# Optimization experiments

Measured on AMD Instinct MI355X. Metric: run time of the kernel, lower is better.

## Reference

```python
import jax, jax.numpy as jnp
import numpy as np

T, N, D, H = 512, 64, 1024, 1024  # time, batch(envs), input dim, hidden dim


def setup_inputs() -> dict:
    key = jax.random.key(0)
    ks = jax.random.split(key, 7)
    x = jax.random.normal(ks[0], (T, N, D), jnp.float32)
    hx = jax.random.normal(ks[1], (N, H), jnp.float32)
    mask = (jax.random.uniform(ks[2], (T, N)) > 0.05).astype(jnp.float32)
    s = float(1.0 / np.sqrt(H))
    w_ih = jax.random.uniform(ks[3], (3 * H, D), jnp.float32, -s, s)
    w_hh = jax.random.uniform(ks[4], (3 * H, H), jnp.float32, -s, s)
    b_ih = jax.random.uniform(ks[5], (3 * H,), jnp.float32, -s, s)
    b_hh = jax.random.uniform(ks[6], (3 * H,), jnp.float32, -s, s)
    return {"x": x, "hx": hx, "mask": mask, "w_ih": w_ih, "w_hh": w_hh,
            "b_ih": b_ih, "b_hh": b_hh}


def reference(x, hx, mask, w_ih, w_hh, b_ih, b_hh):
    """Masked GRU scan, equivalent to the segment-splitting torch loop:
    h is multiplied by mask[t] before every step (mask==1 inside episodes,
    0 at episode boundaries, so this matches masking only at segment starts).
    """
    # Precompute input projections for all timesteps in one big GEMM: [T,N,3H]
    gi = jnp.einsum('tnd,gd->tng', x, w_ih) + b_ih

    def step(h, inp):
        gi_t, m_t = inp                       # [N,3H], [N]
        h = h * m_t[:, None]                  # reset hidden at episode starts
        gh = h @ w_hh.T + b_hh                # [N,3H]
        i_r, i_z, i_n = jnp.split(gi_t, 3, axis=-1)
        h_r, h_z, h_n = jnp.split(gh, 3, axis=-1)
        r = jax.nn.sigmoid(i_r + h_r)
        z = jax.nn.sigmoid(i_z + h_z)
        n = jnp.tanh(i_n + r * h_n)
        h_new = (1.0 - z) * n + z * h
        return h_new, h_new

    h_final, out = jax.lax.scan(step, hx, (gi, mask))
    return out, h_final
```

## Files before the change

kernel.cpp:

```cpp
#include <hip/hip_runtime.h>

#define TT 512
#define NN 64
#define DD 1024
#define HH 1024
#define NSLOT 32

typedef __attribute__((ext_vector_type(8))) short bf16x8;
typedef __attribute__((ext_vector_type(4))) float f32x4;
typedef __attribute__((ext_vector_type(8))) unsigned short u16x8;
typedef __attribute__((ext_vector_type(4))) int i32x4;
typedef __attribute__((ext_vector_type(2))) int i32x2;

__device__ unsigned short g_wih[192u * 2048 * 8];
__device__ unsigned short g_whh[192u * 2048 * 8];
__device__ unsigned short g_x[2048u * 2048 * 8];
__device__ unsigned short g_gi[(size_t)2048 * 64 * 768];
__device__ unsigned g_hbuf32[(size_t)NSLOT * 4 * 16384];

__device__ __forceinline__ unsigned short f2bf(float f) {
  unsigned u = __float_as_uint(f);
  u += 0x7fffu + ((u >> 16) & 1u);
  return (unsigned short)(u >> 16);
}

__global__ void prep_kernel(const float* __restrict__ x,
                            const float* __restrict__ wih,
                            const float* __restrict__ whh) {
  const int gsz = gridDim.x * blockDim.x;
  const int gid = blockIdx.x * blockDim.x + threadIdx.x;
  for (int z = gid; z < NSLOT * 4 * 16384; z += gsz) g_hbuf32[z] = 0u;

  const int W8 = 192 * 2048;
  const int X8 = 2048 * 2048;
  for (int idx = gid; idx < 2 * W8 + X8; idx += gsz) {
    if (idx < 2 * W8) {
      const float* src = (idx < W8) ? wih : whh;
      unsigned short* dst = (idx < W8) ? g_wih : g_whh;
      int i8 = (idx < W8) ? idx : idx - W8;
      size_t g = (size_t)i8 * 8;
      int col = (int)(g >> 10);
      int k = (int)(g & 1023);
      int kk = k >> 5, lg = (k >> 3) & 3;
      int cg = col >> 4;
      int l = (col & 15) | (lg << 4);
      size_t o8 = ((size_t)cg * 32 + kk) * 64 + l;
      const float* p = src + g;
      float4 v0 = *(const float4*)(p);
      float4 v1 = *(const float4*)(p + 4);
      u16x8 u;
      u[0] = f2bf(v0.x); u[1] = f2bf(v0.y); u[2] = f2bf(v0.z); u[3] = f2bf(v0.w);
      u[4] = f2bf(v1.x); u[5] = f2bf(v1.y); u[6] = f2bf(v1.z); u[7] = f2bf(v1.w);
      *(u16x8*)(dst + o8 * 8) = u;
    } else {
      int i8 = idx - 2 * W8;
      size_t g = (size_t)i8 * 8;
      int row = (int)(g >> 10);
      int k = (int)(g & 1023);
      int t = row >> 6, env = row & 63;
      int eg = env >> 4;
      int kk = k >> 5, lg = (k >> 3) & 3;
      int l = (env & 15) | (lg << 4);
      size_t o8 = (((size_t)t * 4 + eg) * 32 + kk) * 64 + l;
      const float* p = x + g;
      float4 v0 = *(const float4*)(p);
      float4 v1 = *(const float4*)(p + 4);
      u16x8 u;
      u[0] = f2bf(v0.x); u[1] = f2bf(v0.y); u[2] = f2bf(v0.z); u[3] = f2bf(v0.w);
      u[4] = f2bf(v1.x); u[5] = f2bf(v1.y); u[6] = f2bf(v1.z); u[7] = f2bf(v1.w);
      *(u16x8*)(g_x + o8 * 8) = u;
    }
  }
}

__global__ __launch_bounds__(256) void gemm_gi() {
  extern __shared__ char smem[];
  unsigned short* As = (unsigned short*)smem;
  unsigned short* Bs = As + 2048 * 8;
  const int tid = threadIdx.x;
  const int bid = blockIdx.x;
  const int mblk = bid & 255, nblk = bid >> 8;
  const int w = tid >> 6, l = tid & 63;
  const int wm = w >> 1, wn = w & 1;

  u16x8 pa[8], pb[8];
  #pragma unroll
  for (int i = 0; i < 8; ++i) {
    int e = tid + i * 256;
    int mt = e >> 8, kkl = (e >> 6) & 3, lane = e & 63;
    pa[i] = *((const u16x8*)g_x  + ((size_t)(mblk * 8 + mt) * 32 + kkl) * 64 + lane);
    pb[i] = *((const u16x8*)g_wih + ((size_t)(nblk * 8 + mt) * 32 + kkl) * 64 + lane);
  }
  f32x4 acc[4][4] = {};
  for (int c = 0; c < 8; ++c) {
    __syncthreads();
    #pragma unroll
    for (int i = 0; i < 8; ++i) {
      int e = tid + i * 256;
      ((u16x8*)As)[e] = pa[i];
      ((u16x8*)Bs)[e] = pb[i];
    }
    __syncthreads();
    if (c < 7) {
      #pragma unroll
      for (int i = 0; i < 8; ++i) {
        int e = tid + i * 256;
        int mt = e >> 8, kkl = (e >> 6) & 3, lane = e & 63;
        pa[i] = *((const u16x8*)g_x  + ((size_t)(mblk * 8 + mt) * 32 + (c + 1) * 4 + kkl) * 64 + lane);
        pb[i] = *((const u16x8*)g_wih + ((size_t)(nblk * 8 + mt) * 32 + (c + 1) * 4 + kkl) * 64 + lane);
      }
    }
    #pragma unroll
    for (int kkl = 0; kkl < 4; ++kkl) {
      bf16x8 af[4], bfr[4];
      #pragma unroll
      for (int ai = 0; ai < 4; ++ai) af[ai]  = ((const bf16x8*)As)[((wm * 4 + ai) * 4 + kkl) * 64 + l];
      #pragma unroll
      for (int bi = 0; bi < 4; ++bi) bfr[bi] = ((const bf16x8*)Bs)[((wn * 4 + bi) * 4 + kkl) * 64 + l];
      #pragma unroll
      for (int ai = 0; ai < 4; ++ai)
        #pragma unroll
        for (int bi = 0; bi < 4; ++bi)
          acc[ai][bi] = __builtin_amdgcn_mfma_f32_16x16x32_bf16(af[ai], bfr[bi], acc[ai][bi], 0, 0, 0);
    }
  }
  const int jj = l & 15;
  #pragma unroll
  for (int ai = 0; ai < 4; ++ai)
    #pragma unroll
    for (int bi = 0; bi < 4; ++bi) {
      int mt = mblk * 8 + wm * 4 + ai;
      int nt = nblk * 8 + wn * 4 + bi;
      int gate = nt >> 6, jg = nt & 63;
      size_t base = ((size_t)mt * 64 + jg) * 768 + (size_t)gate * 256;
      #pragma unroll
      for (int i = 0; i < 4; ++i) {
        int env = (l >> 4) * 4 + i;
        g_gi[base + env * 16 + jj] = f2bf(acc[ai][bi][i]);
      }
    }
}

__global__ __launch_bounds__(256) void scan_kernel(const float* __restrict__ hx,
                                                   const float* __restrict__ mask,
                                                   const float* __restrict__ bih,
                                                   const float* __restrict__ bhh,
                                                   float* __restrict__ out) {
  extern __shared__ char smem[];
  unsigned short* whhL = (unsigned short*)smem;
  unsigned short* hA   = whhL + 3 * 2048 * 8;
  float* Cl = (float*)(hA + 2048 * 8);

  const int tid = threadIdx.x;
  const int bid = blockIdx.x;
  const int eg = (bid & 7) >> 1;
  const int jg = ((bid >> 3) << 1) | (bid & 1);
  const int e0 = eg * 16;
  const int w3 = tid >> 6, l = tid & 63;
  const int e_ = tid >> 4, jj = tid & 15;
  const int j = jg * 16 + jj;

  #pragma unroll 4
  for (int i = 0; i < 24; ++i) {
    int e = tid + i * 256;
    int gate = e >> 11, rem = e & 2047;
    ((u16x8*)whhL)[e] = *((const u16x8*)g_whh + (size_t)(gate * 64 + jg) * 2048 + rem);
  }

  const int kf = jg * 16 + jj;
  const int widx = (((kf >> 5) * 64) + (e_ | (((kf >> 3) & 3) << 4))) * 8 + (kf & 7);

  float hreg;
  {
    float h0 = hx[(size_t)(e0 + e_) * HH + j] * mask[e0 + e_];
    hreg = h0;
    unsigned tw = (1u << 16) | (unsigned)f2bf(h0);
    unsigned* dst = g_hbuf32 + ((size_t)eg << 14) + widx;
    asm volatile("global_store_dword %0, %1, off sc0 sc1" :: "v"(dst), "v"(tw) : "memory");
  }

  const float br  = bih[j] + bhh[j];
  const float bz  = bih[HH + j] + bhh[HH + j];
  const float bin = bih[2 * HH + j];
  const float bhn = bhh[2 * HH + j];

  unsigned short pgr0, pgz0, pgn0, pgr1, pgz1, pgn1;
  {
    size_t gb0 = ((size_t)eg * 64 + jg) * 768;
    pgr0 = g_gi[gb0 + tid]; pgz0 = g_gi[gb0 + 256 + tid]; pgn0 = g_gi[gb0 + 512 + tid];
    size_t gb1 = ((size_t)(4 + eg) * 64 + jg) * 768;
    pgr1 = g_gi[gb1 + tid]; pgz1 = g_gi[gb1 + 256 + tid]; pgn1 = g_gi[gb1 + 512 + tid];
  }

  const unsigned voff = (unsigned)tid * 16;

  for (int t = 0; t < TT; ++t) {
    int tm = (t + 1 < TT) ? (t + 1) : (TT - 1);
    float mnext = mask[tm * NN + e0 + e_];

    const int slot = t & (NSLOT - 1);
    const unsigned* hb = g_hbuf32 + (((size_t)slot * 4 + eg) << 14);
    const unsigned tagc = (unsigned)(t + 1);

    {
      const unsigned* pp = hb + (l << 8);
      while (true) {
        unsigned v;
        asm volatile("global_load_dword %0, %1, off sc0 sc1\n\t"
                     "s_waitcnt vmcnt(0)"
                     : "=v"(v) : "v"(pp) : "memory");
        if (__all((v >> 16) >= tagc)) break;
        __builtin_amdgcn_s_sleep(1);
      }
      __builtin_amdgcn_sched_barrier(0);
    }

    const unsigned tagp = tagc << 16;
    const i32x4* hp = (const i32x4*)hb + tid;
    i32x4 hv[16];
    #pragma unroll
    for (int c = 0; c < 16; ++c) hv[c] = hp[c * 256];

    unsigned stale = 0;
    #pragma unroll
    for (int c = 0; c < 16; ++c) {
      unsigned bad = (((unsigned)hv[c][0] ^ tagp) | ((unsigned)hv[c][1] ^ tagp) |
                      ((unsigned)hv[c][2] ^ tagp) | ((unsigned)hv[c][3] ^ tagp)) & 0xFFFF0000u;
      if (bad) stale |= (1u << c);
      else {
        i32x2 pk;
        pk[0] = (int)__builtin_amdgcn_perm((unsigned)hv[c][1], (unsigned)hv[c][0], 0x05040100u);
        pk[1] = (int)__builtin_amdgcn_perm((unsigned)hv[c][3], (unsigned)hv[c][2], 0x05040100u);
        ((i32x2*)hA)[c * 256 + tid] = pk;
      }
    }
    while (__any(stale != 0)) {
      #pragma unroll
      for (int c = 0; c < 16; ++c) if (stale & (1u << c)) {
        asm volatile("global_load_dwordx4 %0, %1, %2 sc0 sc1"
                     : "=v"(hv[c]) : "v"(voff), "s"((const void*)(hb + c * 1024)));
      }
      asm volatile("s_waitcnt vmcnt(0)" ::: "memory");
      __builtin_amdgcn_sched_barrier(0);
      #pragma unroll
      for (int c = 0; c < 16; ++c) if (stale & (1u << c)) {
        unsigned bad = (((unsigned)hv[c][0] ^ tagp) | ((unsigned)hv[c][1] ^ tagp) |
                        ((unsigned)hv[c][2] ^ tagp) | ((unsigned)hv[c][3] ^ tagp)) & 0xFFFF0000u;
        if (!bad) {
          i32x2 pk;
          pk[0] = (int)__builtin_amdgcn_perm((unsigned)hv[c][1], (unsigned)hv[c][0], 0x05040100u);
          pk[1] = (int)__builtin_amdgcn_perm((unsigned)hv[c][3], (unsigned)hv[c][2], 0x05040100u);
          ((i32x2*)hA)[c * 256 + tid] = pk;
          stale &= ~(1u << c);
        }
      }
    }
    __syncthreads();

    float gr  = __uint_as_float((unsigned)pgr0 << 16);
    float gz  = __uint_as_float((unsigned)pgz0 << 16);
    float gn_ = __uint_as_float((unsigned)pgn0 << 16);
    pgr0 = pgr1; pgz0 = pgz1; pgn0 = pgn1;
    {
      int t2 = (t + 2 < TT) ? (t + 2) : (TT - 1);
      size_t gb = ((size_t)(t2 * 4 + eg) * 64 + jg) * 768;
      pgr1 = g_gi[gb + tid]; pgz1 = g_gi[gb + 256 + tid]; pgn1 = g_gi[gb + 512 + tid];
    }

    if (w3 < 3) {
      const bf16x8* ap = (const bf16x8*)hA;
      const bf16x8* bp = (const bf16x8*)whhL + (size_t)w3 * 2048;
      f32x4 a0 = {0.f,0.f,0.f,0.f}, a1 = {0.f,0.f,0.f,0.f};
      f32x4 a2 = {0.f,0.f,0.f,0.f}, a3 = {0.f,0.f,0.f,0.f};
      #pragma unroll 8
      for (int kk = 0; kk < 8; ++kk) {
        a0 = __builtin_amdgcn_mfma_f32_16x16x32_bf16(ap[kk * 64 + l],        bp[kk * 64 + l],        a0, 0, 0, 0);
        a1 = __builtin_amdgcn_mfma_f32_16x16x32_bf16(ap[(kk + 8) * 64 + l],  bp[(kk + 8) * 64 + l],  a1, 0, 0, 0);
        a2 = __builtin_amdgcn_mfma_f32_16x16x32_bf16(ap[(kk + 16) * 64 + l], bp[(kk + 16) * 64 + l], a2, 0, 0, 0);
        a3 = __builtin_amdgcn_mfma_f32_16x16x32_bf16(ap[(kk + 24) * 64 + l], bp[(kk + 24) * 64 + l], a3, 0, 0, 0);
      }
      f32x4 s;
      #pragma unroll
      for (int i = 0; i < 4; ++i) s[i] = (a0[i] + a1[i]) + (a2[i] + a3[i]);
      int col = l & 15, r0 = (l >> 4) * 4;
      #pragma unroll
      for (int i = 0; i < 4; ++i) Cl[w3 * 256 + (r0 + i) * 16 + col] = s[i];
    }
    __syncthreads();

    {
      float pr = gr + Cl[tid] + br;
      float pz = gz + Cl[256 + tid] + bz;
      float r = 1.f / (1.f + __expf(-pr));
      float z = 1.f / (1.f + __expf(-pz));
      float hn = Cl[512 + tid] + bhn;
      float gn = gn_ + bin + r * hn;
      float e2g = __expf(2.f * gn);
      float n = 1.f - 2.f / (e2g + 1.f);
      float hnew = (1.f - z) * n + z * hreg;

      if (t + 1 < TT) {
        float hm = hnew * mnext;
        hreg = hm;
        unsigned tw = ((unsigned)(t + 2) << 16) | (unsigned)f2bf(hm);
        unsigned* dst = g_hbuf32 + ((((size_t)((t + 1) & (NSLOT - 1))) * 4 + eg) << 14) + widx;
        asm volatile("global_store_dword %0, %1, off sc0 sc1" :: "v"(dst), "v"(tw) : "memory");
      }

      out[(size_t)t * NN * HH + (size_t)(e0 + e_) * HH + j] = hnew;
      if (t == TT - 1)
        out[(size_t)TT * NN * HH + (size_t)(e0 + e_) * HH + j] = hnew;
    }
  }
}

extern "C" void kernel_launch(void* const* d_in, const int* in_sizes, int n_in,
                              void* d_out, int out_size, void* d_ws, size_t ws_size,
                              hipStream_t stream) {
  (void)in_sizes; (void)n_in; (void)d_ws; (void)ws_size; (void)out_size;
  const float* x    = (const float*)d_in[0];
  const float* hx   = (const float*)d_in[1];
  const float* mask = (const float*)d_in[2];
  const float* wih  = (const float*)d_in[3];
  const float* whh  = (const float*)d_in[4];
  const float* bih  = (const float*)d_in[5];
  const float* bhh  = (const float*)d_in[6];
  float* out = (float*)d_out;

  hipFuncSetAttribute((const void*)gemm_gi, hipFuncAttributeMaxDynamicSharedMemorySize, 65536);
  hipFuncSetAttribute((const void*)scan_kernel, hipFuncAttributeMaxDynamicSharedMemorySize, 134144);

  prep_kernel<<<2048, 256, 0, stream>>>(x, wih, whh);
  gemm_gi<<<6144, 256, 65536, stream>>>();
  scan_kernel<<<256, 256, 134144, stream>>>(hx, mask, bih, bhh, out);
}
```

Baseline: 1.929 ms.

## Fuse input projection GEMM into the recurrent scan kernel

Drops the separate gemm_gi kernel and the bf16 g_gi intermediate. Each scan block now keeps its slice of W_ih in registers (32 bf16x8 per lane) and computes the x_t·W_ih^T contribution with MFMAs at the start of every timestep, before it polls for the hidden state. The goal is to hide the input-projection work behind the cross-block synchronisation wait and avoid the global-memory round trip for gi. The cost is much higher register pressure (launch_bounds 256,1), an extra Cl region in shared memory, and fresh reads of x from global memory on every step.

```diff
diff --git a/kernel.cpp b/kernel.cpp
--- a/kernel.cpp
+++ b/kernel.cpp
@@ -15,7 +15,6 @@
 __device__ unsigned short g_wih[192u * 2048 * 8];
 __device__ unsigned short g_whh[192u * 2048 * 8];
 __device__ unsigned short g_x[2048u * 2048 * 8];
-__device__ unsigned short g_gi[(size_t)2048 * 64 * 768];
 __device__ unsigned g_hbuf32[(size_t)NSLOT * 4 * 16384];
 
 __device__ __forceinline__ unsigned short f2bf(float f) {
@@ -73,79 +72,11 @@
   }
 }
 
-__global__ __launch_bounds__(256) void gemm_gi() {
-  extern __shared__ char smem[];
-  unsigned short* As = (unsigned short*)smem;
-  unsigned short* Bs = As + 2048 * 8;
-  const int tid = threadIdx.x;
-  const int bid = blockIdx.x;
-  const int mblk = bid & 255, nblk = bid >> 8;
-  const int w = tid >> 6, l = tid & 63;
-  const int wm = w >> 1, wn = w & 1;
-
-  u16x8 pa[8], pb[8];
-  #pragma unroll
-  for (int i = 0; i < 8; ++i) {
-    int e = tid + i * 256;
-    int mt = e >> 8, kkl = (e >> 6) & 3, lane = e & 63;
-    pa[i] = *((const u16x8*)g_x  + ((size_t)(mblk * 8 + mt) * 32 + kkl) * 64 + lane);
-    pb[i] = *((const u16x8*)g_wih + ((size_t)(nblk * 8 + mt) * 32 + kkl) * 64 + lane);
-  }
-  f32x4 acc[4][4] = {};
-  for (int c = 0; c < 8; ++c) {
-    __syncthreads();
-    #pragma unroll
-    for (int i = 0; i < 8; ++i) {
-      int e = tid + i * 256;
-      ((u16x8*)As)[e] = pa[i];
-      ((u16x8*)Bs)[e] = pb[i];
-    }
-    __syncthreads();
-    if (c < 7) {
-      #pragma unroll
-      for (int i = 0; i < 8; ++i) {
-        int e = tid + i * 256;
-        int mt = e >> 8, kkl = (e >> 6) & 3, lane = e & 63;
-        pa[i] = *((const u16x8*)g_x  + ((size_t)(mblk * 8 + mt) * 32 + (c + 1) * 4 + kkl) * 64 + lane);
-        pb[i] = *((const u16x8*)g_wih + ((size_t)(nblk * 8 + mt) * 32 + (c + 1) * 4 + kkl) * 64 + lane);
-      }
-    }
-    #pragma unroll
-    for (int kkl = 0; kkl < 4; ++kkl) {
-      bf16x8 af[4], bfr[4];
-      #pragma unroll
-      for (int ai = 0; ai < 4; ++ai) af[ai]  = ((const bf16x8*)As)[((wm * 4 + ai) * 4 + kkl) * 64 + l];
-      #pragma unroll
-      for (int bi = 0; bi < 4; ++bi) bfr[bi] = ((const bf16x8*)Bs)[((wn * 4 + bi) * 4 + kkl) * 64 + l];
-      #pragma unroll
-      for (int ai = 0; ai < 4; ++ai)
-        #pragma unroll
-        for (int bi = 0; bi < 4; ++bi)
-          acc[ai][bi] = __builtin_amdgcn_mfma_f32_16x16x32_bf16(af[ai], bfr[bi], acc[ai][bi], 0, 0, 0);
-    }
-  }
-  const int jj = l & 15;
-  #pragma unroll
-  for (int ai = 0; ai < 4; ++ai)
-    #pragma unroll
-    for (int bi = 0; bi < 4; ++bi) {
-      int mt = mblk * 8 + wm * 4 + ai;
-      int nt = nblk * 8 + wn * 4 + bi;
-      int gate = nt >> 6, jg = nt & 63;
-      size_t base = ((size_t)mt * 64 + jg) * 768 + (size_t)gate * 256;
-      #pragma unroll
-      for (int i = 0; i < 4; ++i) {
-        int env = (l >> 4) * 4 + i;
-        g_gi[base + env * 16 + jj] = f2bf(acc[ai][bi][i]);
-      }
-    }
-}
-
-__global__ __launch_bounds__(256) void scan_kernel(const float* __restrict__ hx,
-                                                   const float* __restrict__ mask,
-                                                   const float* __restrict__ bih,
-                                                   const float* __restrict__ bhh,
-                                                   float* __restrict__ out) {
+__global__ __launch_bounds__(256, 1) void scan_kernel(const float* __restrict__ hx,
+                                                      const float* __restrict__ mask,
+                                                      const float* __restrict__ bih,
+                                                      const float* __restrict__ bhh,
+                                                      float* __restrict__ out) {
   extern __shared__ char smem[];
   unsigned short* whhL = (unsigned short*)smem;
   unsigned short* hA   = whhL + 3 * 2048 * 8;
@@ -167,6 +98,13 @@
     ((u16x8*)whhL)[e] = *((const u16x8*)g_whh + (size_t)(gate * 64 + jg) * 2048 + rem);
   }
 
+  bf16x8 wihR[32];
+  if (w3 < 3) {
+    const bf16x8* wp = (const bf16x8*)g_wih + (size_t)(w3 * 64 + jg) * 2048;
+    #pragma unroll
+    for (int kk = 0; kk < 32; ++kk) wihR[kk] = wp[kk * 64 + l];
+  }
+
   const int kf = jg * 16 + jj;
   const int widx = (((kf >> 5) * 64) + (e_ | (((kf >> 3) & 3) << 4))) * 8 + (kf & 7);
 
@@ -184,14 +122,6 @@
   const float bin = bih[2 * HH + j];
   const float bhn = bhh[2 * HH + j];
 
-  unsigned short pgr0, pgz0, pgn0, pgr1, pgz1, pgn1;
-  {
-    size_t gb0 = ((size_t)eg * 64 + jg) * 768;
-    pgr0 = g_gi[gb0 + tid]; pgz0 = g_gi[gb0 + 256 + tid]; pgn0 = g_gi[gb0 + 512 + tid];
-    size_t gb1 = ((size_t)(4 + eg) * 64 + jg) * 768;
-    pgr1 = g_gi[gb1 + tid]; pgz1 = g_gi[gb1 + 256 + tid]; pgn1 = g_gi[gb1 + 512 + tid];
-  }
-
   const unsigned voff = (unsigned)tid * 16;
 
   for (int t = 0; t < TT; ++t) {
@@ -201,6 +131,17 @@
     const int slot = t & (NSLOT - 1);
     const unsigned* hb = g_hbuf32 + (((size_t)slot * 4 + eg) << 14);
     const unsigned tagc = (unsigned)(t + 1);
+
+    f32x4 xa0 = {0.f,0.f,0.f,0.f}, xa1 = {0.f,0.f,0.f,0.f};
+    if (w3 < 3) {
+      const bf16x8* xp = (const bf16x8*)g_x + (size_t)(t * 4 + eg) * 2048;
+      #pragma unroll
+      for (int kk = 0; kk < 16; ++kk) {
+        xa0 = __builtin_amdgcn_mfma_f32_16x16x32_bf16(xp[kk * 64 + l],        wihR[kk],      xa0, 0, 0, 0);
+        xa1 = __builtin_amdgcn_mfma_f32_16x16x32_bf16(xp[(kk + 16) * 64 + l], wihR[kk + 16], xa1, 0, 0, 0);
+      }
+    }
+    __builtin_amdgcn_sched_barrier(0);
 
     {
       const unsigned* pp = hb + (l << 8);
@@ -257,16 +198,6 @@
     }
     __syncthreads();
 
-    float gr  = __uint_as_float((unsigned)pgr0 << 16);
-    float gz  = __uint_as_float((unsigned)pgz0 << 16);
-    float gn_ = __uint_as_float((unsigned)pgn0 << 16);
-    pgr0 = pgr1; pgz0 = pgz1; pgn0 = pgn1;
-    {
-      int t2 = (t + 2 < TT) ? (t + 2) : (TT - 1);
-      size_t gb = ((size_t)(t2 * 4 + eg) * 64 + jg) * 768;
-      pgr1 = g_gi[gb + tid]; pgz1 = g_gi[gb + 256 + tid]; pgn1 = g_gi[gb + 512 + tid];
-    }
-
     if (w3 < 3) {
       const bf16x8* ap = (const bf16x8*)hA;
       const bf16x8* bp = (const bf16x8*)whhL + (size_t)w3 * 2048;
@@ -279,22 +210,28 @@
         a2 = __builtin_amdgcn_mfma_f32_16x16x32_bf16(ap[(kk + 16) * 64 + l], bp[(kk + 16) * 64 + l], a2, 0, 0, 0);
         a3 = __builtin_amdgcn_mfma_f32_16x16x32_bf16(ap[(kk + 24) * 64 + l], bp[(kk + 24) * 64 + l], a3, 0, 0, 0);
       }
-      f32x4 s;
-      #pragma unroll
-      for (int i = 0; i < 4; ++i) s[i] = (a0[i] + a1[i]) + (a2[i] + a3[i]);
       int col = l & 15, r0 = (l >> 4) * 4;
-      #pragma unroll
-      for (int i = 0; i < 4; ++i) Cl[w3 * 256 + (r0 + i) * 16 + col] = s[i];
+      if (w3 < 2) {
+        #pragma unroll
+        for (int i = 0; i < 4; ++i)
+          Cl[w3 * 256 + (r0 + i) * 16 + col] = (xa0[i] + xa1[i]) + ((a0[i] + a1[i]) + (a2[i] + a3[i]));
+      } else {
+        #pragma unroll
+        for (int i = 0; i < 4; ++i) {
+          Cl[2 * 256 + (r0 + i) * 16 + col] = xa0[i] + xa1[i];
+          Cl[3 * 256 + (r0 + i) * 16 + col] = (a0[i] + a1[i]) + (a2[i] + a3[i]);
+        }
+      }
     }
     __syncthreads();
 
     {
-      float pr = gr + Cl[tid] + br;
-      float pz = gz + Cl[256 + tid] + bz;
+      float pr = Cl[tid] + br;
+      float pz = Cl[256 + tid] + bz;
       float r = 1.f / (1.f + __expf(-pr));
       float z = 1.f / (1.f + __expf(-pz));
-      float hn = Cl[512 + tid] + bhn;
-      float gn = gn_ + bin + r * hn;
+      float hn = Cl[768 + tid] + bhn;
+      float gn = Cl[512 + tid] + bin + r * hn;
       float e2g = __expf(2.f * gn);
       float n = 1.f - 2.f / (e2g + 1.f);
       float hnew = (1.f - z) * n + z * hreg;
@@ -327,10 +264,8 @@
   const float* bhh  = (const float*)d_in[6];
   float* out = (float*)d_out;
 
-  hipFuncSetAttribute((const void*)gemm_gi, hipFuncAttributeMaxDynamicSharedMemorySize, 65536);
-  hipFuncSetAttribute((const void*)scan_kernel, hipFuncAttributeMaxDynamicSharedMemorySize, 134144);
+  hipFuncSetAttribute((const void*)scan_kernel, hipFuncAttributeMaxDynamicSharedMemorySize, 135168);
 
   prep_kernel<<<2048, 256, 0, stream>>>(x, wih, whh);
-  gemm_gi<<<6144, 256, 65536, stream>>>();
-  scan_kernel<<<256, 256, 134144, stream>>>(hx, mask, bih, bhh, out);
-}
+  scan_kernel<<<256, 256, 135168, stream>>>(hx, mask, bih, bhh, out);
+}
```

Measured after the change: 3.274 ms. 1.7x slower.
